# Kernel optimization log

Hardware: AMD Instinct MI355X
Metric: run time of the kernel (lower is better)

Reference implementation:

```python
import jax, jax.numpy as jnp
import numpy as np

N_NODES = 50000
NEG_SLOPE = 0.2  # PyG GATConv default
EPS = 1e-16      # PyG softmax denominator epsilon


def _gat_conv(x, edge_index, W, att_src, att_dst, bias):
    """Single-head PyG-style GATConv with self-loops.
    x: [N, F_in], edge_index: [2, E] (row 0 = src/j, row 1 = dst/i).
    """
    n = x.shape[0]
    loop = jnp.arange(n, dtype=edge_index.dtype)
    src = jnp.concatenate([edge_index[0], loop])  # [E+N]
    dst = jnp.concatenate([edge_index[1], loop])  # [E+N]

    h = x @ W                                      # [N, F_out]
    a_src = h @ att_src                            # [N]
    a_dst = h @ att_dst                            # [N]

    e = jax.nn.leaky_relu(a_src[src] + a_dst[dst], NEG_SLOPE)  # [E+N]
    # segment softmax over incoming edges of each dst node
    m = jax.ops.segment_max(e, dst, num_segments=n)
    m = jnp.where(jnp.isfinite(m), m, 0.0)
    e = jnp.exp(e - m[dst])
    s = jax.ops.segment_sum(e, dst, num_segments=n)
    alpha = e / (s[dst] + EPS)                     # [E+N]

    out = jax.ops.segment_sum(alpha[:, None] * h[src], dst, num_segments=n)
    return out + bias


def setup_inputs() -> dict:
    key = jax.random.key(0)
    ks = jax.random.split(key, 10)
    d_in, d_hid, d_emb = 128, 64, 64
    n_edges = 800000
    x = jax.random.normal(ks[0], (N_NODES, d_in), dtype=jnp.float32)
    edge_index = jax.random.randint(ks[1], (2, n_edges), 0, N_NODES, dtype=jnp.int64)
    def glorot(k, shape):
        lim = float(np.sqrt(6.0 / sum(shape)))
        return jax.random.uniform(k, shape, jnp.float32, -lim, lim)
    return {
        "x": x,
        "edge_index": edge_index,
        "W1": glorot(ks[2], (d_in, d_hid)),
        "att_src1": glorot(ks[3], (d_hid,)),
        "att_dst1": glorot(ks[4], (d_hid,)),
        "b1": jnp.zeros((d_hid,), jnp.float32),
        "W2": glorot(ks[5], (d_hid, d_emb)),
        "att_src2": glorot(ks[6], (d_emb,)),
        "att_dst2": glorot(ks[7], (d_emb,)),
        "b2": jnp.zeros((d_emb,), jnp.float32),
    }


def reference(x, edge_index, W1, att_src1, att_dst1, b1, W2, att_src2, att_dst2, b2):
    x1 = jax.nn.relu(_gat_conv(x, edge_index, W1, att_src1, att_dst1, b1))
    # dropout is identity in eval mode
    x2 = _gat_conv(x1, edge_index, W2, att_src2, att_dst2, b2)
    return x2
```

## Files before the change

### kernel.cpp

```cpp
#include <hip/hip_runtime.h>
#include <hip/hip_bf16.h>

#define F_OUT 64
#define NEG_SLOPE 0.2f
#define SOFT_EPS 1e-16f
#define BW 256
#define CH 8192
#define TH 512
#define TH3 512

typedef short short8 __attribute__((ext_vector_type(8)));
typedef float floatx4 __attribute__((ext_vector_type(4)));
typedef unsigned short ushort8v __attribute__((ext_vector_type(8)));
typedef long long ll2 __attribute__((ext_vector_type(2)));
typedef int int2v __attribute__((ext_vector_type(2)));

__device__ __forceinline__ unsigned short f2bf_bits(float v) {
    __hip_bfloat16 hb = __float2bfloat16(v);
    return *(unsigned short*)&hb;
}
__device__ __forceinline__ float bf_bits2f(unsigned short u) {
    __hip_bfloat16 hb = *(__hip_bfloat16*)&u;
    return __bfloat162float(hb);
}
__device__ __forceinline__ float read_any(const void* src, int off, int bf) {
    return bf ? __bfloat162float(((const __hip_bfloat16*)src)[off])
              : ((const float*)src)[off];
}
__device__ __forceinline__ int get_idx(const void* ei, int i64, long long pos) {
    return i64 ? (int)((const long long*)ei)[pos] : ((const int*)ei)[pos];
}

__device__ __forceinline__ void detect_local(const unsigned* wbits, const unsigned* ebits,
                                             int* sm_bf, int* sm_i64) {
    if (threadIdx.x < 64) {
        unsigned w = wbits[threadIdx.x];
        unsigned e = (w >> 7) & 0xFFu;
        unsigned long long mb = __ballot(e >= 0x60u && e <= 0x7Eu);
        unsigned long long mz = __ballot(ebits[2 * threadIdx.x + 1] == 0u);
        if (threadIdx.x == 0) { *sm_bf = (__popcll(mb) > 32); *sm_i64 = (__popcll(mz) > 32); }
    }
    __syncthreads();
}

__device__ __forceinline__ void load_idx2(const void* ei, int i64, long long base, int t,
                                          int* v0, int* v1) {
    if (i64) {
        ll2 d = *(const ll2*)((const long long*)ei + base + t);
        *v0 = (int)d[0]; *v1 = (int)d[1];
    } else {
        int2v d = *(const int2v*)((const int*)ei + base + t);
        *v0 = d[0]; *v1 = d[1];
    }
}

__global__ void count_prep(const void* __restrict__ ei, int* __restrict__ table,
                           const void* w1, const void* as1, const void* ad1, const void* b1,
                           const void* w2, const void* as2, const void* ad2, const void* b2,
                           unsigned short* __restrict__ wt1, unsigned short* __restrict__ wt2,
                           float* __restrict__ vecs, int* __restrict__ flags,
                           int E, int total, int NB, int nchunks, int n1, int n2, int K1) {
    __shared__ int cnt[1024];
    __shared__ int s_bf, s_i64;
    detect_local((const unsigned*)w1, (const unsigned*)ei, &s_bf, &s_i64);
    int bf = s_bf, i64 = s_i64;
    int g = blockIdx.x, tid = threadIdx.x;
    if (g == 0 && tid == 0) { flags[0] = bf; flags[1] = i64; }

    if (g < nchunks) {
        for (int k = tid; k < NB; k += TH) cnt[k] = 0;
        __syncthreads();
        int base = g * CH;
        int lim = base + CH < total ? base + CH : total;
        int elim = lim < E ? lim : E;
        for (int t = base + tid * 2; t < elim; t += TH * 2) {
            if (t + 1 < elim) {
                int i0, i1;
                load_idx2(ei, i64, (long long)E, t, &i0, &i1);
                atomicAdd(&cnt[i0 >> 8], 1);
                atomicAdd(&cnt[i1 >> 8], 1);
            } else {
                int i0 = get_idx(ei, i64, (long long)E + t);
                atomicAdd(&cnt[i0 >> 8], 1);
            }
        }
        for (int t = (base > E ? base : E) + tid; t < lim; t += TH)
            atomicAdd(&cnt[(t - E) >> 8], 1);
        __syncthreads();
        for (int k = tid; k < NB; k += TH) table[k * nchunks + g] = cnt[k];
    } else {
        int wtotal = n1 + n2 + 384;
        for (int t = tid; t < wtotal; t += TH) {
            if (t < n1) {
                int n = t / K1, k = t - n * K1;
                wt1[t] = f2bf_bits(read_any(w1, k * F_OUT + n, bf));
            } else if (t < n1 + n2) {
                int u = t - n1;
                int n = u >> 6, k = u & 63;
                wt2[u] = f2bf_bits(read_any(w2, k * F_OUT + n, bf));
            } else {
                int u = t - n1 - n2;
                const void* srcp[6] = {as1, ad1, b1, as2, ad2, b2};
                vecs[u] = read_any(srcp[u >> 6], u & 63, bf);
            }
        }
    }
}

template <int K, int WAVES>
__device__ __forceinline__ void gemm_body(int blk, int tid,
                          const void* __restrict__ xv, const unsigned short* __restrict__ Wt,
                          const float* __restrict__ att_s, const float* __restrict__ att_d,
                          unsigned short* __restrict__ h, float* __restrict__ a_s,
                          float* __restrict__ a_d, int N, int bf) {
    int lane = tid & 63;
    int m0 = (blk * WAVES + (tid >> 6)) * 16;
    if (m0 >= N) return;
    int c = lane & 15, quad = lane >> 4;
    int arow = m0 + c;
    if (arow >= N) arow = N - 1;

    floatx4 acc0 = {0.f, 0.f, 0.f, 0.f};
    floatx4 acc1 = acc0, acc2 = acc0, acc3 = acc0;

    for (int kc = 0; kc < K; kc += 32) {
        int ka = kc + quad * 8;
        short8 a;
        if (bf) {
            a = *(const short8*)((const unsigned short*)xv + (size_t)arow * K + ka);
        } else {
            const float* xp = (const float*)xv + (size_t)arow * K + ka;
            floatx4 f0 = *(const floatx4*)xp;
            floatx4 f1 = *(const floatx4*)(xp + 4);
#pragma unroll
            for (int j = 0; j < 4; ++j) {
                a[j]     = (short)f2bf_bits(f0[j]);
                a[4 + j] = (short)f2bf_bits(f1[j]);
            }
        }
        short8 b0 = *(const short8*)(Wt + (size_t)(c)      * K + ka);
        short8 b1 = *(const short8*)(Wt + (size_t)(16 + c) * K + ka);
        short8 b2 = *(const short8*)(Wt + (size_t)(32 + c) * K + ka);
        short8 b3 = *(const short8*)(Wt + (size_t)(48 + c) * K + ka);
        acc0 = __builtin_amdgcn_mfma_f32_16x16x32_bf16(a, b0, acc0, 0, 0, 0);
        acc1 = __builtin_amdgcn_mfma_f32_16x16x32_bf16(a, b1, acc1, 0, 0, 0);
        acc2 = __builtin_amdgcn_mfma_f32_16x16x32_bf16(a, b2, acc2, 0, 0, 0);
        acc3 = __builtin_amdgcn_mfma_f32_16x16x32_bf16(a, b3, acc3, 0, 0, 0);
    }

    float as0 = att_s[c],      as1 = att_s[16 + c], as2 = att_s[32 + c], as3 = att_s[48 + c];
    float ad0 = att_d[c],      ad1 = att_d[16 + c], ad2 = att_d[32 + c], ad3 = att_d[48 + c];
#pragma unroll
    for (int reg = 0; reg < 4; ++reg) {
        int row = m0 + quad * 4 + reg;
        float vs = acc0[reg] * as0 + acc1[reg] * as1 + acc2[reg] * as2 + acc3[reg] * as3;
        float vd = acc0[reg] * ad0 + acc1[reg] * ad1 + acc2[reg] * ad2 + acc3[reg] * ad3;
#pragma unroll
        for (int off = 1; off < 16; off <<= 1) {
            vs += __shfl_xor(vs, off);
            vd += __shfl_xor(vd, off);
        }
        if (row < N) {
            if (c == 0) { a_s[row] = vs; a_d[row] = vd; }
            unsigned short* hr = h + (size_t)row * F_OUT + c;
            hr[0]  = f2bf_bits(acc0[reg]);
            hr[16] = f2bf_bits(acc1[reg]);
            hr[32] = f2bf_bits(acc2[reg]);
            hr[48] = f2bf_bits(acc3[reg]);
        }
    }
}

__global__ void __launch_bounds__(TH)
scatter_gemm1(const void* __restrict__ ei, const int* __restrict__ table,
              unsigned* __restrict__ staged, int* __restrict__ segbeg,
              int* __restrict__ row_ptr, const void* __restrict__ xv,
              const unsigned short* __restrict__ Wt,
              const float* __restrict__ att_s, const float* __restrict__ att_d,
              unsigned short* __restrict__ h, float* __restrict__ a_s,
              float* __restrict__ a_d, const unsigned* __restrict__ wbits,
              int E, int total, int NB, int nchunks, int N) {
    __shared__ int s_bf, s_i64;
    detect_local(wbits, (const unsigned*)ei, &s_bf, &s_i64);
    int tid = threadIdx.x;
    if ((int)blockIdx.x >= nchunks) {
        gemm_body<128, 8>(blockIdx.x - nchunks, tid, xv, Wt, att_s, att_d,
                          h, a_s, a_d, N, s_bf);
        return;
    }
    __shared__ int s_scan[TH];
    __shared__ int s_cur[1024];
    int g = blockIdx.x;
    int i64 = s_i64;
    int b0 = 0;
    if (tid < NB) {
        const int* row = table + (size_t)tid * nchunks;
        int rsum = 0, rpart = 0;
        for (int c2 = 0; c2 < nchunks; ++c2) {
            int v = row[c2];
            rsum += v;
            rpart += (c2 < g) ? v : 0;
        }
        b0 = rsum;
        s_cur[tid] = rpart;
    }
    s_scan[tid] = (tid < NB) ? b0 : 0;
    __syncthreads();
    for (int off = 1; off < TH; off <<= 1) {
        int v = (tid >= off) ? s_scan[tid - off] : 0;
        __syncthreads();
        s_scan[tid] += v;
        __syncthreads();
    }
    if (tid < NB) {
        int excl = s_scan[tid] - b0;
        s_cur[tid] = excl + s_cur[tid];
        if (g == 0) segbeg[tid] = excl;
    }
    if (g == 0 && tid == 0) { segbeg[NB] = total; row_ptr[N] = total; }
    __syncthreads();
    int base = g * CH;
    int lim = base + CH < total ? base + CH : total;
    int elim = lim < E ? lim : E;
    for (int t = base + tid * 2; t < elim; t += TH * 2) {
        if (t + 1 < elim) {
            int j0, j1, i0, i1;
            load_idx2(ei, i64, 0, t, &j0, &j1);
            load_idx2(ei, i64, (long long)E, t, &i0, &i1);
            int pos0 = atomicAdd(&s_cur[i0 >> 8], 1);
            staged[pos0] = ((unsigned)(i0 & 255) << 24) | (unsigned)j0;
            int pos1 = atomicAdd(&s_cur[i1 >> 8], 1);
            staged[pos1] = ((unsigned)(i1 & 255) << 24) | (unsigned)j1;
        } else {
            int j0 = get_idx(ei, i64, t);
            int i0 = get_idx(ei, i64, (long long)E + t);
            int pos0 = atomicAdd(&s_cur[i0 >> 8], 1);
            staged[pos0] = ((unsigned)(i0 & 255) << 24) | (unsigned)j0;
        }
    }
    for (int t = (base > E ? base : E) + tid; t < lim; t += TH) {
        int v = t - E;
        int pos = atomicAdd(&s_cur[v >> 8], 1);
        staged[pos] = ((unsigned)(v & 255) << 24) | (unsigned)v;
    }
}

__global__ void __launch_bounds__(TH3)
bucket_csr(const unsigned* __restrict__ staged, const int* __restrict__ segbeg,
           int* __restrict__ row_ptr, int* __restrict__ eidx, int N) {
    __shared__ int ldeg[BW];
    __shared__ int lcur[BW];
    __shared__ int wtot[4];
    int b = blockIdx.x;
    int t = threadIdx.x;
    int seg_beg = segbeg[b];
    int seg_end = segbeg[b + 1];
    if (t < BW) ldeg[t] = 0;
    __syncthreads();
    for (int p = seg_beg + t; p < seg_end; p += TH3)
        atomicAdd(&ldeg[staged[p] >> 24], 1);
    __syncthreads();
    int lane = t & 63, w = t >> 6;
    int d = 0, v = 0;
    if (t < BW) {
        d = ldeg[t];
        v = d;
#pragma unroll
        for (int off = 1; off < 64; off <<= 1) {
            int u = __shfl_up(v, off);
            if (lane >= off) v += u;
        }
        if (lane == 63) wtot[w] = v;
    }
    __syncthreads();
    if (t < BW) {
        int woff = 0;
        for (int k = 0; k < w; ++k) woff += wtot[k];
        int excl = v - d + woff;
        int node = b * BW + t;
        if (node < N) row_ptr[node] = seg_beg + excl;
        lcur[t] = excl;
    }
    __syncthreads();
    for (int p = seg_beg + t; p < seg_end; p += TH3) {
        unsigned pk = staged[p];
        int pos = atomicAdd(&lcur[pk >> 24], 1);
        eidx[seg_beg + pos] = (int)(pk & 0xFFFFFFu);
    }
}

__device__ __forceinline__ void gather_node8x2(int ia, int ib, int grp, int c8,
                                               const int* __restrict__ row_ptr,
                                               const int* __restrict__ eidx,
                                               const float* __restrict__ a_s,
                                               const float* __restrict__ a_d,
                                               const unsigned short* __restrict__ h,
                                               float* sea_out, float acca[8],
                                               float* seb_out, float accb[8], int N) {
    const char* hb8 = (const char*)h;
    unsigned cofs = (unsigned)(c8 << 4);
    int bega = row_ptr[ia], enda = row_ptr[ia + 1];
    int lena = enda - bega;
    float ada = a_d[ia];
    int pa = bega + ((lena * grp) >> 3);
    int gea = bega + ((lena * (grp + 1)) >> 3);
    int pb = 0, geb = 0;
    float adb = 0.f;
    if (ib < N) {
        int begb = row_ptr[ib], endb = row_ptr[ib + 1];
        int lenb = endb - begb;
        adb = a_d[ib];
        pb = begb + ((lenb * grp) >> 3);
        geb = begb + ((lenb * (grp + 1)) >> 3);
    }
    float sea = 0.f, seb = 0.f;
#pragma unroll
    for (int k = 0; k < 8; ++k) { acca[k] = 0.f; accb[k] = 0.f; }

    while (pa < gea || pb < geb) {
        bool va0 = pa < gea, va1 = pa + 1 < gea;
        bool vb0 = pb < geb, vb1 = pb + 1 < geb;
        int ja0 = va0 ? eidx[pa]     : 0;
        int ja1 = va1 ? eidx[pa + 1] : 0;
        int jb0 = vb0 ? eidx[pb]     : 0;
        int jb1 = vb1 ? eidx[pb + 1] : 0;
        ushort8v ha0 = *(const ushort8v*)(hb8 + (((unsigned)ja0 << 7) + cofs));
        ushort8v ha1 = *(const ushort8v*)(hb8 + (((unsigned)ja1 << 7) + cofs));
        ushort8v hb0 = *(const ushort8v*)(hb8 + (((unsigned)jb0 << 7) + cofs));
        ushort8v hb1 = *(const ushort8v*)(hb8 + (((unsigned)jb1 << 7) + cofs));
        float ea0 = a_s[ja0] + ada;
        float ea1 = a_s[ja1] + ada;
        float eb0 = a_s[jb0] + adb;
        float eb1 = a_s[jb1] + adb;
        float wa0 = va0 ? __expf(fmaxf(ea0, NEG_SLOPE * ea0)) : 0.f;
        float wa1 = va1 ? __expf(fmaxf(ea1, NEG_SLOPE * ea1)) : 0.f;
        float wb0 = vb0 ? __expf(fmaxf(eb0, NEG_SLOPE * eb0)) : 0.f;
        float wb1 = vb1 ? __expf(fmaxf(eb1, NEG_SLOPE * eb1)) : 0.f;
        sea += wa0 + wa1;
        seb += wb0 + wb1;
#pragma unroll
        for (int k = 0; k < 8; ++k) {
            acca[k] += wa0 * bf_bits2f(ha0[k]) + wa1 * bf_bits2f(ha1[k]);
            accb[k] += wb0 * bf_bits2f(hb0[k]) + wb1 * bf_bits2f(hb1[k]);
        }
        pa += 2; pb += 2;
    }

#pragma unroll
    for (int off = 8; off < 64; off <<= 1) {
        sea += __shfl_xor(sea, off);
        seb += __shfl_xor(seb, off);
#pragma unroll
        for (int k = 0; k < 8; ++k) {
            acca[k] += __shfl_xor(acca[k], off);
            accb[k] += __shfl_xor(accb[k], off);
        }
    }
    *sea_out = sea;
    *seb_out = seb;
}

#define XST 72
__global__ void __launch_bounds__(512)
gather1_gemm2(const int* __restrict__ row_ptr, const int* __restrict__ eidx,
              const float* __restrict__ a_s, const float* __restrict__ a_d,
              const unsigned short* __restrict__ h, const float* __restrict__ bias,
              const unsigned short* __restrict__ Wt2,
              const float* __restrict__ att_s2, const float* __restrict__ att_d2,
              unsigned short* __restrict__ h2, float* __restrict__ a_s2,
              float* __restrict__ a_d2, int N) {
    __shared__ unsigned short x1t[16 * XST];
    int tid = threadIdx.x;
    int lane = tid & 63;
    int wv = tid >> 6;
    int grp = lane >> 3, c8 = lane & 7;
    int ia = blockIdx.x * 16 + (wv << 1);
    int ib = ia + 1;

    if (ia < N) {
        float sea, seb, acca[8], accb[8];
        gather_node8x2(ia, ib, grp, c8, row_ptr, eidx, a_s, a_d, h,
                       &sea, acca, &seb, accb, N);
        if (grp == 0) {
            int col = c8 << 3;
            float inv = 1.f / (sea + SOFT_EPS);
            ushort8v ov;
#pragma unroll
            for (int k = 0; k < 8; ++k) {
                float v = acca[k] * inv + bias[col + k];
                ov[k] = f2bf_bits(v > 0.f ? v : 0.f);
            }
            *(ushort8v*)(x1t + (wv * 2) * XST + col) = ov;
            if (ib < N) {
                inv = 1.f / (seb + SOFT_EPS);
#pragma unroll
                for (int k = 0; k < 8; ++k) {
                    float v = accb[k] * inv + bias[col + k];
                    ov[k] = f2bf_bits(v > 0.f ? v : 0.f);
                }
            } else {
                ov = (ushort8v){0, 0, 0, 0, 0, 0, 0, 0};
            }
            *(ushort8v*)(x1t + (wv * 2 + 1) * XST + col) = ov;
        }
    } else if (grp == 0) {
        *(ushort8v*)(x1t + (wv * 2)     * XST + (c8 << 3)) = (ushort8v){0, 0, 0, 0, 0, 0, 0, 0};
        *(ushort8v*)(x1t + (wv * 2 + 1) * XST + (c8 << 3)) = (ushort8v){0, 0, 0, 0, 0, 0, 0, 0};
    }
    __syncthreads();

    if (wv == 0) {
        int quad = lane >> 4, c = lane & 15;
        int m0 = blockIdx.x * 16;
        floatx4 acc0 = {0.f, 0.f, 0.f, 0.f};
        floatx4 acc1 = acc0, acc2 = acc0, acc3 = acc0;
#pragma unroll
        for (int kc = 0; kc < 64; kc += 32) {
            int ka = kc + quad * 8;
            short8 a = *(const short8*)(x1t + c * XST + ka);
            short8 b0 = *(const short8*)(Wt2 + (size_t)(c)      * 64 + ka);
            short8 b1 = *(const short8*)(Wt2 + (size_t)(16 + c) * 64 + ka);
            short8 b2 = *(const short8*)(Wt2 + (size_t)(32 + c) * 64 + ka);
            short8 b3 = *(const short8*)(Wt2 + (size_t)(48 + c) * 64 + ka);
            acc0 = __builtin_amdgcn_mfma_f32_16x16x32_bf16(a, b0, acc0, 0, 0, 0);
            acc1 = __builtin_amdgcn_mfma_f32_16x16x32_bf16(a, b1, acc1, 0, 0, 0);
            acc2 = __builtin_amdgcn_mfma_f32_16x16x32_bf16(a, b2, acc2, 0, 0, 0);
            acc3 = __builtin_amdgcn_mfma_f32_16x16x32_bf16(a, b3, acc3, 0, 0, 0);
        }
        float as0 = att_s2[c],      as1 = att_s2[16 + c], as2 = att_s2[32 + c], as3 = att_s2[48 + c];
        float ad0 = att_d2[c],      ad1 = att_d2[16 + c], ad2 = att_d2[32 + c], ad3 = att_d2[48 + c];
#pragma unroll
        for (int reg = 0; reg < 4; ++reg) {
            int row = m0 + quad * 4 + reg;
            float vs = acc0[reg] * as0 + acc1[reg] * as1 + acc2[reg] * as2 + acc3[reg] * as3;
            float vd = acc0[reg] * ad0 + acc1[reg] * ad1 + acc2[reg] * ad2 + acc3[reg] * ad3;
#pragma unroll
            for (int off = 1; off < 16; off <<= 1) {
                vs += __shfl_xor(vs, off);
                vd += __shfl_xor(vd, off);
            }
            if (row < N) {
                if (c == 0) { a_s2[row] = vs; a_d2[row] = vd; }
                unsigned short* hr = h2 + (size_t)row * F_OUT + c;
                hr[0]  = f2bf_bits(acc0[reg]);
                hr[16] = f2bf_bits(acc1[reg]);
                hr[32] = f2bf_bits(acc2[reg]);
                hr[48] = f2bf_bits(acc3[reg]);
            }
        }
    }
}

__global__ void __launch_bounds__(256)
node_gather_out(const int* __restrict__ row_ptr, const int* __restrict__ eidx,
                const float* __restrict__ a_s, const float* __restrict__ a_d,
                const unsigned short* __restrict__ h, const float* __restrict__ bias,
                void* __restrict__ out, int N, const int* __restrict__ flags) {
    int lane = threadIdx.x & 63;
    int wv = threadIdx.x >> 6;
    int ia = blockIdx.x * 8 + (wv << 1);
    int ib = ia + 1;
    if (ia >= N) return;
    int grp = lane >> 3, c8 = lane & 7;
    float sea, seb, acca[8], accb[8];
    gather_node8x2(ia, ib, grp, c8, row_ptr, eidx, a_s, a_d, h,
                   &sea, acca, &seb, accb, N);
    if (grp == 0) {
        int col = c8 << 3;
        int obf = flags[0];
#pragma unroll
        for (int nn = 0; nn < 2; ++nn) {
            int i = nn ? ib : ia;
            if (i >= N) break;
            float se = nn ? seb : sea;
            const float* ac = nn ? accb : acca;
            float inv = 1.f / (se + SOFT_EPS);
            float v[8];
#pragma unroll
            for (int k = 0; k < 8; ++k) v[k] = ac[k] * inv + bias[col + k];
            size_t o = (size_t)i * F_OUT + col;
            if (obf) {
                ushort8v ov;
#pragma unroll
                for (int k = 0; k < 8; ++k) ov[k] = f2bf_bits(v[k]);
                *(ushort8v*)((unsigned short*)out + o) = ov;
            } else {
                floatx4 o0 = {v[0], v[1], v[2], v[3]};
                floatx4 o1 = {v[4], v[5], v[6], v[7]};
                *(floatx4*)((float*)out + o) = o0;
                *(floatx4*)((float*)out + o + 4) = o1;
            }
        }
    }
}

extern "C" void kernel_launch(void* const* d_in, const int* in_sizes, int n_in,
                              void* d_out, int out_size, void* d_ws, size_t ws_size,
                              hipStream_t stream) {
    const void* x   = d_in[0];
    const void* ei  = d_in[1];
    const void* W1  = d_in[2];
    const void* as1 = d_in[3];
    const void* ad1 = d_in[4];
    const void* b1  = d_in[5];
    const void* W2  = d_in[6];
    const void* as2 = d_in[7];
    const void* ad2 = d_in[8];
    const void* b2  = d_in[9];

    int E  = in_sizes[1] / 2;
    int n1 = in_sizes[2];
    int n2 = in_sizes[6];
    int K1 = n1 / F_OUT;
    int N  = in_sizes[0] / K1;
    int total = E + N;
    int NB = (N + BW - 1) / BW;
    int nchunks = (total + CH - 1) / CH;
    int M = NB * nchunks;

    size_t nf = (size_t)N * F_OUT;
    char* wsb = (char*)d_ws;
    unsigned short* h   = (unsigned short*)wsb;
    unsigned short* h2  = h + nf;
    unsigned short* wt1 = h2 + nf;
    unsigned short* wt2 = wt1 + n1;
    float* a_s  = (float*)(wt2 + n2 + ((n1 + n2) & 1));
    float* a_d  = a_s + N;
    float* a_s2 = a_d + N;
    float* a_d2 = a_s2 + N;
    float* vecs = a_d2 + N;
    float* cAs1 = vecs,       *cAd1 = vecs + 64,  *cB1 = vecs + 128;
    float* cAs2 = vecs + 192, *cAd2 = vecs + 256, *cB2 = vecs + 320;
    int* flags    = (int*)(vecs + 384);
    int* row_ptr  = flags + 8;
    int* eidx     = row_ptr + N + 1;
    unsigned* staged = (unsigned*)(eidx + total);
    int* table    = (int*)(staged + total);
    int* segbeg   = table + M;

    int blkG1 = (N + 127) / 128;
    int blkFuse = (N + 15) / 16;
    int blkNode = (N + 7) / 8;

    count_prep<<<nchunks + 1, TH, 0, stream>>>(ei, table, W1, as1, ad1, b1,
                                               W2, as2, ad2, b2, wt1, wt2, vecs, flags,
                                               E, total, NB, nchunks, n1, n2, K1);
    scatter_gemm1<<<nchunks + blkG1, TH, 0, stream>>>(ei, table, staged, segbeg, row_ptr,
                                                      x, wt1, cAs1, cAd1, h, a_s, a_d,
                                                      (const unsigned*)W1,
                                                      E, total, NB, nchunks, N);
    bucket_csr<<<NB, TH3, 0, stream>>>(staged, segbeg, row_ptr, eidx, N);
    gather1_gemm2<<<blkFuse, 512, 0, stream>>>(row_ptr, eidx, a_s, a_d, h, cB1,
                                               wt2, cAs2, cAd2, h2, a_s2, a_d2, N);
    node_gather_out<<<blkNode, 256, 0, stream>>>(row_ptr, eidx, a_s2, a_d2, h2, cB2,
                                                 d_out, N, flags);
}
```

Measured before the change: 179.1 us.

## Split edge gathers into two feature-half passes to shrink gather working set

Each neighbor-aggregation kernel now gathers only 32 of the 64 bf16 features per pass (8-byte loads instead of 16-byte) and runs twice, once per half. The first layer writes its low half to a workspace buffer that the fused GEMM kernel reads back. The intent is to shrink the random-access footprint of h per pass so it fits better in cache. In exchange, edge indices, attention scalars and exp weights are recomputed in every pass, there are extra launches, and an intermediate buffer makes a round trip.

```diff
diff --git a/kernel.cpp b/kernel.cpp
--- a/kernel.cpp
+++ b/kernel.cpp
@@ -12,6 +12,7 @@
 typedef short short8 __attribute__((ext_vector_type(8)));
 typedef float floatx4 __attribute__((ext_vector_type(4)));
 typedef unsigned short ushort8v __attribute__((ext_vector_type(8)));
+typedef unsigned short ushort4v __attribute__((ext_vector_type(4)));
 typedef long long ll2 __attribute__((ext_vector_type(2)));
 typedef int int2v __attribute__((ext_vector_type(2)));
 
@@ -289,16 +290,16 @@
     }
 }
 
-__device__ __forceinline__ void gather_node8x2(int ia, int ib, int grp, int c8,
+__device__ __forceinline__ void gather_half8x2(int ia, int ib, int grp, int c8, int phase,
                                                const int* __restrict__ row_ptr,
                                                const int* __restrict__ eidx,
                                                const float* __restrict__ a_s,
                                                const float* __restrict__ a_d,
                                                const unsigned short* __restrict__ h,
-                                               float* sea_out, float acca[8],
-                                               float* seb_out, float accb[8], int N) {
+                                               float* sea_out, float acca[4],
+                                               float* seb_out, float accb[4], int N) {
     const char* hb8 = (const char*)h;
-    unsigned cofs = (unsigned)(c8 << 4);
+    unsigned cofs = ((unsigned)phase << 6) + ((unsigned)c8 << 3);
     int bega = row_ptr[ia], enda = row_ptr[ia + 1];
     int lena = enda - bega;
     float ada = a_d[ia];
@@ -315,7 +316,7 @@
     }
     float sea = 0.f, seb = 0.f;
 #pragma unroll
-    for (int k = 0; k < 8; ++k) { acca[k] = 0.f; accb[k] = 0.f; }
+    for (int k = 0; k < 4; ++k) { acca[k] = 0.f; accb[k] = 0.f; }
 
     while (pa < gea || pb < geb) {
         bool va0 = pa < gea, va1 = pa + 1 < gea;
@@ -324,10 +325,10 @@
         int ja1 = va1 ? eidx[pa + 1] : 0;
         int jb0 = vb0 ? eidx[pb]     : 0;
         int jb1 = vb1 ? eidx[pb + 1] : 0;
-        ushort8v ha0 = *(const ushort8v*)(hb8 + (((unsigned)ja0 << 7) + cofs));
-        ushort8v ha1 = *(const ushort8v*)(hb8 + (((unsigned)ja1 << 7) + cofs));
-        ushort8v hb0 = *(const ushort8v*)(hb8 + (((unsigned)jb0 << 7) + cofs));
-        ushort8v hb1 = *(const ushort8v*)(hb8 + (((unsigned)jb1 << 7) + cofs));
+        ushort4v ha0 = *(const ushort4v*)(hb8 + (((unsigned)ja0 << 7) + cofs));
+        ushort4v ha1 = *(const ushort4v*)(hb8 + (((unsigned)ja1 << 7) + cofs));
+        ushort4v hb0 = *(const ushort4v*)(hb8 + (((unsigned)jb0 << 7) + cofs));
+        ushort4v hb1 = *(const ushort4v*)(hb8 + (((unsigned)jb1 << 7) + cofs));
         float ea0 = a_s[ja0] + ada;
         float ea1 = a_s[ja1] + ada;
         float eb0 = a_s[jb0] + adb;
@@ -339,7 +340,7 @@
         sea += wa0 + wa1;
         seb += wb0 + wb1;
 #pragma unroll
-        for (int k = 0; k < 8; ++k) {
+        for (int k = 0; k < 4; ++k) {
             acca[k] += wa0 * bf_bits2f(ha0[k]) + wa1 * bf_bits2f(ha1[k]);
             accb[k] += wb0 * bf_bits2f(hb0[k]) + wb1 * bf_bits2f(hb1[k]);
         }
@@ -351,7 +352,7 @@
         sea += __shfl_xor(sea, off);
         seb += __shfl_xor(seb, off);
 #pragma unroll
-        for (int k = 0; k < 8; ++k) {
+        for (int k = 0; k < 4; ++k) {
             acca[k] += __shfl_xor(acca[k], off);
             accb[k] += __shfl_xor(accb[k], off);
         }
@@ -360,15 +361,52 @@
     *seb_out = seb;
 }
 
+__global__ void __launch_bounds__(256)
+gather1_p0(const int* __restrict__ row_ptr, const int* __restrict__ eidx,
+           const float* __restrict__ a_s, const float* __restrict__ a_d,
+           const unsigned short* __restrict__ h, const float* __restrict__ bias,
+           unsigned short* __restrict__ x1lo, int N) {
+    int lane = threadIdx.x & 63;
+    int wv = threadIdx.x >> 6;
+    int ia = blockIdx.x * 8 + (wv << 1);
+    int ib = ia + 1;
+    if (ia >= N) return;
+    int grp = lane >> 3, c8 = lane & 7;
+    float sea, seb, acca[4], accb[4];
+    gather_half8x2(ia, ib, grp, c8, 0, row_ptr, eidx, a_s, a_d, h,
+                   &sea, acca, &seb, accb, N);
+    if (grp == 0) {
+        int col = c8 << 2;
+        float inv = 1.f / (sea + SOFT_EPS);
+        ushort4v ov;
+#pragma unroll
+        for (int k = 0; k < 4; ++k) {
+            float v = acca[k] * inv + bias[col + k];
+            ov[k] = f2bf_bits(v > 0.f ? v : 0.f);
+        }
+        *(ushort4v*)(x1lo + (size_t)ia * 32 + col) = ov;
+        if (ib < N) {
+            inv = 1.f / (seb + SOFT_EPS);
+#pragma unroll
+            for (int k = 0; k < 4; ++k) {
+                float v = accb[k] * inv + bias[col + k];
+                ov[k] = f2bf_bits(v > 0.f ? v : 0.f);
+            }
+            *(ushort4v*)(x1lo + (size_t)ib * 32 + col) = ov;
+        }
+    }
+}
+
 #define XST 72
 __global__ void __launch_bounds__(512)
-gather1_gemm2(const int* __restrict__ row_ptr, const int* __restrict__ eidx,
-              const float* __restrict__ a_s, const float* __restrict__ a_d,
-              const unsigned short* __restrict__ h, const float* __restrict__ bias,
-              const unsigned short* __restrict__ Wt2,
-              const float* __restrict__ att_s2, const float* __restrict__ att_d2,
-              unsigned short* __restrict__ h2, float* __restrict__ a_s2,
-              float* __restrict__ a_d2, int N) {
+gather1_p1(const int* __restrict__ row_ptr, const int* __restrict__ eidx,
+           const float* __restrict__ a_s, const float* __restrict__ a_d,
+           const unsigned short* __restrict__ h, const float* __restrict__ bias,
+           const unsigned short* __restrict__ x1lo,
+           const unsigned short* __restrict__ Wt2,
+           const float* __restrict__ att_s2, const float* __restrict__ att_d2,
+           unsigned short* __restrict__ h2, float* __restrict__ a_s2,
+           float* __restrict__ a_d2, int N) {
     __shared__ unsigned short x1t[16 * XST];
     int tid = threadIdx.x;
     int lane = tid & 63;
@@ -378,34 +416,43 @@
     int ib = ia + 1;
 
     if (ia < N) {
-        float sea, seb, acca[8], accb[8];
-        gather_node8x2(ia, ib, grp, c8, row_ptr, eidx, a_s, a_d, h,
+        float sea, seb, acca[4], accb[4];
+        gather_half8x2(ia, ib, grp, c8, 1, row_ptr, eidx, a_s, a_d, h,
                        &sea, acca, &seb, accb, N);
         if (grp == 0) {
-            int col = c8 << 3;
+            int col = c8 << 2;
+            ushort4v lo = *(const ushort4v*)(x1lo + (size_t)ia * 32 + col);
+            *(ushort4v*)(x1t + (wv * 2) * XST + col) = lo;
             float inv = 1.f / (sea + SOFT_EPS);
-            ushort8v ov;
-#pragma unroll
-            for (int k = 0; k < 8; ++k) {
-                float v = acca[k] * inv + bias[col + k];
+            ushort4v ov;
+#pragma unroll
+            for (int k = 0; k < 4; ++k) {
+                float v = acca[k] * inv + bias[32 + col + k];
                 ov[k] = f2bf_bits(v > 0.f ? v : 0.f);
             }
-            *(ushort8v*)(x1t + (wv * 2) * XST + col) = ov;
+            *(ushort4v*)(x1t + (wv * 2) * XST + 32 + col) = ov;
             if (ib < N) {
+                lo = *(const ushort4v*)(x1lo + (size_t)ib * 32 + col);
                 inv = 1.f / (seb + SOFT_EPS);
 #pragma unroll
-                for (int k = 0; k < 8; ++k) {
-                    float v = accb[k] * inv + bias[col + k];
+                for (int k = 0; k < 4; ++k) {
+                    float v = accb[k] * inv + bias[32 + col + k];
                     ov[k] = f2bf_bits(v > 0.f ? v : 0.f);
                 }
             } else {
-                ov = (ushort8v){0, 0, 0, 0, 0, 0, 0, 0};
-            }
-            *(ushort8v*)(x1t + (wv * 2 + 1) * XST + col) = ov;
+                lo = (ushort4v){0, 0, 0, 0};
+                ov = (ushort4v){0, 0, 0, 0};
+            }
+            *(ushort4v*)(x1t + (wv * 2 + 1) * XST + col) = lo;
+            *(ushort4v*)(x1t + (wv * 2 + 1) * XST + 32 + col) = ov;
         }
     } else if (grp == 0) {
-        *(ushort8v*)(x1t + (wv * 2)     * XST + (c8 << 3)) = (ushort8v){0, 0, 0, 0, 0, 0, 0, 0};
-        *(ushort8v*)(x1t + (wv * 2 + 1) * XST + (c8 << 3)) = (ushort8v){0, 0, 0, 0, 0, 0, 0, 0};
+        ushort4v z = (ushort4v){0, 0, 0, 0};
+        int col = c8 << 2;
+        *(ushort4v*)(x1t + (wv * 2)     * XST + col) = z;
+        *(ushort4v*)(x1t + (wv * 2)     * XST + 32 + col) = z;
+        *(ushort4v*)(x1t + (wv * 2 + 1) * XST + col) = z;
+        *(ushort4v*)(x1t + (wv * 2 + 1) * XST + 32 + col) = z;
     }
     __syncthreads();
 
@@ -452,21 +499,21 @@
 }
 
 __global__ void __launch_bounds__(256)
-node_gather_out(const int* __restrict__ row_ptr, const int* __restrict__ eidx,
-                const float* __restrict__ a_s, const float* __restrict__ a_d,
-                const unsigned short* __restrict__ h, const float* __restrict__ bias,
-                void* __restrict__ out, int N, const int* __restrict__ flags) {
+node_gather_half(const int* __restrict__ row_ptr, const int* __restrict__ eidx,
+                 const float* __restrict__ a_s, const float* __restrict__ a_d,
+                 const unsigned short* __restrict__ h, const float* __restrict__ bias,
+                 void* __restrict__ out, int N, const int* __restrict__ flags, int phase) {
     int lane = threadIdx.x & 63;
     int wv = threadIdx.x >> 6;
     int ia = blockIdx.x * 8 + (wv << 1);
     int ib = ia + 1;
     if (ia >= N) return;
     int grp = lane >> 3, c8 = lane & 7;
-    float sea, seb, acca[8], accb[8];
-    gather_node8x2(ia, ib, grp, c8, row_ptr, eidx, a_s, a_d, h,
+    float sea, seb, acca[4], accb[4];
+    gather_half8x2(ia, ib, grp, c8, phase, row_ptr, eidx, a_s, a_d, h,
                    &sea, acca, &seb, accb, N);
     if (grp == 0) {
-        int col = c8 << 3;
+        int col = (phase << 5) + (c8 << 2);
         int obf = flags[0];
 #pragma unroll
         for (int nn = 0; nn < 2; ++nn) {
@@ -475,20 +522,18 @@
             float se = nn ? seb : sea;
             const float* ac = nn ? accb : acca;
             float inv = 1.f / (se + SOFT_EPS);
-            float v[8];
-#pragma unroll
-            for (int k = 0; k < 8; ++k) v[k] = ac[k] * inv + bias[col + k];
+            float v[4];
+#pragma unroll
+            for (int k = 0; k < 4; ++k) v[k] = ac[k] * inv + bias[col + k];
             size_t o = (size_t)i * F_OUT + col;
             if (obf) {
-                ushort8v ov;
-#pragma unroll
-                for (int k = 0; k < 8; ++k) ov[k] = f2bf_bits(v[k]);
-                *(ushort8v*)((unsigned short*)out + o) = ov;
+                ushort4v ov;
+#pragma unroll
+                for (int k = 0; k < 4; ++k) ov[k] = f2bf_bits(v[k]);
+                *(ushort4v*)((unsigned short*)out + o) = ov;
             } else {
                 floatx4 o0 = {v[0], v[1], v[2], v[3]};
-                floatx4 o1 = {v[4], v[5], v[6], v[7]};
                 *(floatx4*)((float*)out + o) = o0;
-                *(floatx4*)((float*)out + o + 4) = o1;
             }
         }
     }
@@ -537,10 +582,13 @@
     unsigned* staged = (unsigned*)(eidx + total);
     int* table    = (int*)(staged + total);
     int* segbeg   = table + M;
+    char* xp = (char*)(segbeg + NB + 1);
+    xp = (char*)(((size_t)xp + 15) & ~(size_t)15);
+    unsigned short* x1lo = (unsigned short*)xp;
 
     int blkG1 = (N + 127) / 128;
-    int blkFuse = (N + 15) / 16;
-    int blkNode = (N + 7) / 8;
+    int blkP0 = (N + 7) / 8;
+    int blkP1 = (N + 15) / 16;
 
     count_prep<<<nchunks + 1, TH, 0, stream>>>(ei, table, W1, as1, ad1, b1,
                                                W2, as2, ad2, b2, wt1, wt2, vecs, flags,
@@ -550,8 +598,11 @@
                                                       (const unsigned*)W1,
                                                       E, total, NB, nchunks, N);
     bucket_csr<<<NB, TH3, 0, stream>>>(staged, segbeg, row_ptr, eidx, N);
-    gather1_gemm2<<<blkFuse, 512, 0, stream>>>(row_ptr, eidx, a_s, a_d, h, cB1,
-                                               wt2, cAs2, cAd2, h2, a_s2, a_d2, N);
-    node_gather_out<<<blkNode, 256, 0, stream>>>(row_ptr, eidx, a_s2, a_d2, h2, cB2,
-                                                 d_out, N, flags);
-}
+    gather1_p0<<<blkP0, 256, 0, stream>>>(row_ptr, eidx, a_s, a_d, h, cB1, x1lo, N);
+    gather1_p1<<<blkP1, 512, 0, stream>>>(row_ptr, eidx, a_s, a_d, h, cB1, x1lo,
+                                          wt2, cAs2, cAd2, h2, a_s2, a_d2, N);
+    node_gather_half<<<blkP0, 256, 0, stream>>>(row_ptr, eidx, a_s2, a_d2, h2, cB2,
+                                                d_out, N, flags, 0);
+    node_gather_half<<<blkP0, 256, 0, stream>>>(row_ptr, eidx, a_s2, a_d2, h2, cB2,
+                                                d_out, N, flags, 1);
+}
```

New measurement: 208.5 us. +16.4%, slower.
